# Performance work log

Hardware: AMD Instinct MI355X
Metric: run time of the kernel (lower is better)

## Reference

```python
import jax, jax.numpy as jnp
import numpy as np

B, T, V, E, H = 64, 512, 8192, 1024, 2048


def setup_inputs() -> dict:
    key = jax.random.key(0)
    k = jax.random.split(key, 8)
    idx = jax.random.randint(k[0], (B, T), 0, V)
    targets = jax.random.randint(k[1], (B, T), 0, V)
    s = 0.02
    W_E = jax.random.normal(k[2], (V, E), jnp.float32) * s
    start = jnp.zeros((1, H), jnp.float32)
    W_xh = jax.random.normal(k[3], (E + H, H), jnp.float32) * s  # Linear(E+H -> H)
    b_xh = jnp.zeros((H,), jnp.float32)
    W_head = jax.random.normal(k[4], (H, V), jnp.float32) * s
    b_head = jnp.zeros((V,), jnp.float32)
    return {"idx": idx, "targets": targets, "W_E": W_E, "start": start,
            "W_xh": W_xh, "b_xh": b_xh, "W_head": W_head, "b_head": b_head}


def reference(idx, targets, W_E, start, W_xh, b_xh, W_head, b_head):
    b, t = idx.shape
    emb = W_E[idx]  # [B, T, E]
    # split concat-linear: cat([x,h]) @ W_xh == x @ Wx + h @ Wh (same math)
    Wx, Wh = W_xh[:E], W_xh[E:]
    xproj = jnp.einsum('bte,eh->bth', emb, Wx) + b_xh  # precompute input part

    def step(h_prev, xp_t):
        h_t = jnp.tanh(xp_t + h_prev @ Wh)
        return h_t, h_t

    h0 = jnp.broadcast_to(start, (b, H))
    _, hs = jax.lax.scan(step, h0, jnp.swapaxes(xproj, 0, 1))  # [T, B, H]
    hidden = jnp.swapaxes(hs, 0, 1)  # [B, T, H]
    logits = jnp.einsum('bth,hv->btv', hidden, W_head) + b_head

    # cross entropy with ignore_index=-1
    logp = jax.nn.log_softmax(logits, axis=-1)
    mask = targets != -1
    tsafe = jnp.where(mask, targets, 0)
    nll = -jnp.take_along_axis(logp, tsafe[..., None], axis=-1)[..., 0]
    loss = jnp.sum(nll * mask) / jnp.maximum(jnp.sum(mask), 1)
    return logits, loss
```

## Files before the change

### kernel.cpp

```cpp
#include <hip/hip_runtime.h>
#include <hip/hip_bf16.h>
#include <math.h>
#include <stdint.h>

#define Bb 64
#define Tt 512
#define Vv 8192
#define Ee 1024
#define Hh 2048

typedef unsigned short u16;
typedef unsigned long long u64;
typedef __attribute__((ext_vector_type(8))) short bf16x8;
typedef __attribute__((ext_vector_type(8))) _Float16 f16x8;
typedef __attribute__((ext_vector_type(4))) float f32x4;

__device__ __forceinline__ u16 f2b(float f) {
  unsigned u = __float_as_uint(f);
  u += 0x7FFF + ((u >> 16) & 1);
  return (u16)(u >> 16);
}
__device__ __forceinline__ float b2f(u16 h) {
  return __uint_as_float(((unsigned)h) << 16);
}
__device__ __forceinline__ u16 f2h_bits(float f) {
  union { _Float16 h; u16 u; } c;
  c.h = (_Float16)f;
  return c.u;
}
__device__ __forceinline__ u64 pack4(u16 a, u16 b, u16 c, u16 d) {
  return (u64)a | ((u64)b << 16) | ((u64)c << 32) | ((u64)d << 48);
}

__device__ __forceinline__ void gload16f(f16x8& dst, const void* addr) {
  asm volatile("global_load_dwordx4 %0, %1, off sc1"
               : "=v"(dst) : "v"(addr) : "memory");
}

__device__ __forceinline__ void gll16(const u16* g, const u16* l) {
  __builtin_amdgcn_global_load_lds((__attribute__((address_space(1))) void*)g,
                                   (__attribute__((address_space(3))) void*)l, 16, 0, 0);
}

__device__ __forceinline__ float wave_max(float v) {
  #pragma unroll
  for (int d = 32; d; d >>= 1) v = fmaxf(v, __shfl_xor(v, d, 64));
  return v;
}
__device__ __forceinline__ float wave_sum(float v) {
  #pragma unroll
  for (int d = 32; d; d >>= 1) v += __shfl_xor(v, d, 64);
  return v;
}


__global__ __launch_bounds__(256)
void embed_cast_f16(const float* __restrict__ WE, const int* __restrict__ idx,
                    u16* __restrict__ emb) {
  const int m = blockIdx.x;
  const int row = idx[m];
  const float4 v = ((const float4*)(WE + (size_t)row * Ee))[threadIdx.x];
  ushort4 o;
  o.x = f2h_bits(v.x); o.y = f2h_bits(v.y);
  o.z = f2h_bits(v.z); o.w = f2h_bits(v.w);
  ((ushort4*)(emb + (size_t)m * Ee))[threadIdx.x] = o;
}

__global__ __launch_bounds__(256)
void transpose_cast(const float* __restrict__ src, u16* __restrict__ dst,
                    int R, int C) {
  __shared__ float tile[32][33];
  const int bi = blockIdx.x;
  const int bj = blockIdx.y;
  const int tid = threadIdx.x;
  const int r  = tid >> 3;
  const int c4 = (tid & 7) * 4;
  float4 v = *(const float4*)(src + (size_t)(bj * 32 + r) * C + bi * 32 + c4);
  tile[r][c4 + 0] = v.x; tile[r][c4 + 1] = v.y;
  tile[r][c4 + 2] = v.z; tile[r][c4 + 3] = v.w;
  __syncthreads();
  ushort4 o;
  o.x = f2b(tile[c4 + 0][r]); o.y = f2b(tile[c4 + 1][r]);
  o.z = f2b(tile[c4 + 2][r]); o.w = f2b(tile[c4 + 3][r]);
  *(ushort4*)(dst + (size_t)(bi * 32 + r) * R + bj * 32 + c4) = o;
}

__global__ __launch_bounds__(256)
void transpose_cast_f16(const float* __restrict__ src, u16* __restrict__ dst,
                        int R, int C) {
  __shared__ float tile[32][33];
  const int bi = blockIdx.x;
  const int bj = blockIdx.y;
  const int tid = threadIdx.x;
  const int r  = tid >> 3;
  const int c4 = (tid & 7) * 4;
  float4 v = *(const float4*)(src + (size_t)(bj * 32 + r) * C + bi * 32 + c4);
  tile[r][c4 + 0] = v.x; tile[r][c4 + 1] = v.y;
  tile[r][c4 + 2] = v.z; tile[r][c4 + 3] = v.w;
  __syncthreads();
  ushort4 o;
  o.x = f2h_bits(tile[c4 + 0][r]); o.y = f2h_bits(tile[c4 + 1][r]);
  o.z = f2h_bits(tile[c4 + 2][r]); o.w = f2h_bits(tile[c4 + 3][r]);
  *(ushort4*)(dst + (size_t)(bi * 32 + r) * R + bj * 32 + c4) = o;
}

__global__ __launch_bounds__(256)
void h0_init(const float* __restrict__ start, u16* __restrict__ hbuf) {
  const int b = blockIdx.x;
  #pragma unroll
  for (int j = 0; j < 8; ++j) {
    int n = threadIdx.x * 8 + j;
    hbuf[(size_t)b * 2048 + n] = f2h_bits(start[n]);
  }
}

template <int MODE, int F16>
__global__ __launch_bounds__(256, 2)
void gemm_bt(const u16* __restrict__ A, const u16* __restrict__ Bt,
             const float* __restrict__ bias, void* __restrict__ outp,
             float* __restrict__ pm, float* __restrict__ ps,
             int M, int N, int K) {
  __shared__ u16 ldsA[128 * 32];
  __shared__ u16 ldsB[128 * 32];
  __shared__ float sm_[2][2][64];
  __shared__ float ss_[2][2][64];
  const int tid = threadIdx.x;
  const int lane = tid & 63;
  const int w = tid >> 6;
  const int wr = w >> 1, wc = w & 1;

  const int nwg = gridDim.x * gridDim.y;
  const int lin = blockIdx.y * gridDim.x + blockIdx.x;
  const int swz = (lin & 7) * (nwg >> 3) + (lin >> 3);
  const int bm = swz % gridDim.x;
  const int bn = swz / gridDim.x;

  const int srow = w * 32 + (lane >> 2);
  const int scol = (lane & 3) * 8;
  const u16* a0 = A + (size_t)(bm * 128 + srow) * K + scol;
  const u16* b0 = Bt + (size_t)(bn * 128 + srow) * K + scol;
  u16* lA0 = ldsA + w * 1024;
  u16* lA1 = ldsA + w * 1024 + 512;
  u16* lB0 = ldsB + w * 1024;
  u16* lB1 = ldsB + w * 1024 + 512;

  f32x4 acc[4][4];
  #pragma unroll
  for (int m = 0; m < 4; ++m)
    #pragma unroll
    for (int n = 0; n < 4; ++n)
      acc[m][n] = (f32x4){0.f, 0.f, 0.f, 0.f};

  const int nk = K >> 5;
  for (int kt = 0; kt < nk; ++kt) {
    __syncthreads();
    const u16* ak = a0 + kt * 32;
    const u16* bk = b0 + kt * 32;
    gll16(ak, lA0);
    gll16(ak + 16 * (size_t)K, lA1);
    gll16(bk, lB0);
    gll16(bk + 16 * (size_t)K, lB1);
    __syncthreads();
    bf16x8 af[4], bfr[4];
    #pragma unroll
    for (int i = 0; i < 4; ++i) {
      af[i]  = *(const bf16x8*)&ldsA[(wr * 64 + i * 16 + (lane & 15)) * 32 + (lane >> 4) * 8];
      bfr[i] = *(const bf16x8*)&ldsB[(wc * 64 + i * 16 + (lane & 15)) * 32 + (lane >> 4) * 8];
    }
    #pragma unroll
    for (int m = 0; m < 4; ++m)
      #pragma unroll
      for (int n = 0; n < 4; ++n) {
        if (F16) {
          acc[m][n] = __builtin_amdgcn_mfma_f32_16x16x32_f16(
              *(const f16x8*)&af[m], *(const f16x8*)&bfr[n], acc[m][n], 0, 0, 0);
        } else {
          acc[m][n] = __builtin_amdgcn_mfma_f32_16x16x32_bf16(af[m], bfr[n], acc[m][n], 0, 0, 0);
        }
      }
  }

  const int r0 = bm * 128 + wr * 64 + (lane >> 4) * 4;
  const int c0 = bn * 128 + wc * 64 + (lane & 15);

  if (MODE == 0) {
    float bv[4];
    #pragma unroll
    for (int n = 0; n < 4; ++n) bv[n] = bias[c0 + n * 16];
    #pragma unroll
    for (int m = 0; m < 4; ++m) {
      #pragma unroll
      for (int q = 0; q < 4; ++q) {
        const int row = r0 + m * 16 + q;
        float v[4];
        float mx = -1e30f;
        #pragma unroll
        for (int n = 0; n < 4; ++n) {
          v[n] = acc[m][n][q] + bv[n];
          ((float*)outp)[(size_t)row * N + c0 + n * 16] = v[n];
          mx = fmaxf(mx, v[n]);
        }
        #pragma unroll
        for (int d = 1; d < 16; d <<= 1) mx = fmaxf(mx, __shfl_xor(mx, d, 64));
        float se = 0.f;
        #pragma unroll
        for (int n = 0; n < 4; ++n) se += expf(v[n] - mx);
        #pragma unroll
        for (int d = 1; d < 16; d <<= 1) se += __shfl_xor(se, d, 64);
        if ((lane & 15) == 0) {
          const int rl = m * 16 + (lane >> 4) * 4 + q;
          sm_[wc][wr][rl] = mx;
          ss_[wc][wr][rl] = se;
        }
      }
    }
    __syncthreads();
    if (w < 2) {
      float m0 = sm_[0][w][lane], m1 = sm_[1][w][lane];
      float s0 = ss_[0][w][lane], s1 = ss_[1][w][lane];
      float Mx = fmaxf(m0, m1);
      float S = s0 * expf(m0 - Mx) + s1 * expf(m1 - Mx);
      const int row = bm * 128 + w * 64 + lane;
      pm[(size_t)row * 64 + bn] = Mx;
      ps[(size_t)row * 64 + bn] = S;
    }
  } else {
    #pragma unroll
    for (int n = 0; n < 4; ++n) {
      const int col = c0 + n * 16;
      const float bv = bias[col];
      #pragma unroll
      for (int m = 0; m < 4; ++m) {
        #pragma unroll
        for (int q = 0; q < 4; ++q) {
          const int row = r0 + m * 16 + q;
          float v = acc[m][n][q] + bv;
          const int b = row >> 9, t = row & 511;
          ((u16*)outp)[((size_t)t * Bb + b) * N + col] = f2b(v);
        }
      }
    }
  }
}

__global__ __launch_bounds__(512, 2)
void rnn_scan(const u16* __restrict__ WhT, const u16* __restrict__ xp,
              u16* __restrict__ hbuf, u16* __restrict__ hidden,
              unsigned* __restrict__ sync) {
  __shared__ u16 whi[65536];
  __shared__ float red[4096];

  const int bid = blockIdx.x;
  const int g = bid >> 6;
  const int colg = bid & 63;
  const int rowbase = g * 16;
  const int col0 = colg * 32;
  const int tid = threadIdx.x;
  const int lane = tid & 63;
  const int w = tid >> 6;

  for (int i = tid; i < 8192; i += 512) {
    const int ch = i & 3;
    const int cl = (i >> 2) & 15;
    const int kt = (i >> 6) & 63;
    const int c2 = (i >> 12) & 1;
    bf16x8 v = *(const bf16x8*)(WhT + (size_t)(col0 + c2 * 16 + cl) * 2048 + kt * 32 + ch * 8);
    *(bf16x8*)&whi[(size_t)(c2 * 64 + kt) * 512 + ch * 128 + cl * 8] = v;
  }
  __syncthreads();

  unsigned* cnt = sync + g * 64;
  bool dead = false;
  const int hrow = rowbase + (lane & 15);

  ushort4 xv = {0, 0, 0, 0};
  if (w < 2)
    xv = *(const ushort4*)(xp + (size_t)hrow * 2048 + col0 + w * 16 + (lane >> 4) * 4);

  for (int t = 0; t < Tt; ++t) {
    const u16* hp = hbuf + (size_t)(t & 1) * (64 * 2048);
    u16*       hn = hbuf + (size_t)((t + 1) & 1) * (64 * 2048);

    f16x8 qh[8];
    const u16* hb = hp + (size_t)hrow * 2048 + (lane >> 4) * 8;
    #pragma unroll
    for (int kt = 0; kt < 8; ++kt)
      gload16f(qh[kt], hb + (w * 8 + kt) * 32);
    asm volatile("s_waitcnt vmcnt(0)" ::: "memory");
    __builtin_amdgcn_sched_barrier(0);

    f32x4 a0 = (f32x4){0.f, 0.f, 0.f, 0.f};
    f32x4 a1 = (f32x4){0.f, 0.f, 0.f, 0.f};
    #pragma unroll
    for (int kt = 0; kt < 8; ++kt) {
      const int ktG = w * 8 + kt;
      f16x8 w0 = *(const f16x8*)&whi[(size_t)(0 * 64 + ktG) * 512 + (lane >> 4) * 128 + (lane & 15) * 8];
      f16x8 w1 = *(const f16x8*)&whi[(size_t)(1 * 64 + ktG) * 512 + (lane >> 4) * 128 + (lane & 15) * 8];
      a0 = __builtin_amdgcn_mfma_f32_16x16x32_f16(w0, qh[kt], a0, 0, 0, 0);
      a1 = __builtin_amdgcn_mfma_f32_16x16x32_f16(w1, qh[kt], a1, 0, 0, 0);
    }

    *(f32x4*)&red[(w) * 256 + lane * 4]     = a0;
    *(f32x4*)&red[(8 + w) * 256 + lane * 4] = a1;
    __syncthreads();

    if (w < 2) {
      f32x4 ac = (f32x4){0.f, 0.f, 0.f, 0.f};
      #pragma unroll
      for (int j = 0; j < 8; ++j)
        ac += *(const f32x4*)&red[(w * 8 + j) * 256 + lane * 4];
      const int cl0 = (lane >> 4) * 4;
      u16 hf[4], hbv[4];
      #pragma unroll
      for (int qq = 0; qq < 4; ++qq) {
        float v = tanhf(ac[qq] + b2f(((const u16*)&xv)[qq]));
        hf[qq]  = f2h_bits(v);
        hbv[qq] = f2b(v);
      }
      u64 ph = pack4(hf[0], hf[1], hf[2], hf[3]);
      u64 pb = pack4(hbv[0], hbv[1], hbv[2], hbv[3]);
      u16* hd = hn + (size_t)hrow * 2048 + col0 + w * 16 + cl0;
      __hip_atomic_store((u64*)hd, ph, __ATOMIC_RELAXED, __HIP_MEMORY_SCOPE_AGENT);
      *(u64*)(hidden + ((size_t)hrow * Tt + t) * Hh + col0 + w * 16 + cl0) = pb;
    }

    __syncthreads();
    if (w < 2 && t + 1 < Tt)
      xv = *(const ushort4*)(xp + ((size_t)(t + 1) * Bb + hrow) * 2048 + col0 + w * 16 + (lane >> 4) * 4);
    if (tid == 0) {
      unsigned old = __hip_atomic_fetch_add(cnt, 1u, __ATOMIC_RELAXED, __HIP_MEMORY_SCOPE_AGENT);
      if (old != (unsigned)(t * 64 + 63) && !dead) {
        unsigned polls = 0;
        while (__hip_atomic_load(cnt, __ATOMIC_RELAXED, __HIP_MEMORY_SCOPE_AGENT)
               < (unsigned)((t + 1) * 64)) {
          if (++polls > 4000000u) { dead = true; break; }
        }
      }
    }
    __syncthreads();
  }
}


__global__ __launch_bounds__(256)
void nll_from_partials(const float* __restrict__ pm, const float* __restrict__ ps,
                       const float* __restrict__ logits, const int* __restrict__ tgt,
                       float* __restrict__ nll) {
  const int r = blockIdx.x * 4 + (threadIdx.x >> 6);
  const int lane = threadIdx.x & 63;
  float m = pm[(size_t)r * 64 + lane];
  float s = ps[(size_t)r * 64 + lane];
  float M = wave_max(m);
  float S = wave_sum(s * expf(m - M));
  if (lane == 0) {
    const int tg = tgt[r];
    float o = 0.f;
    if (tg != -1) o = M + logf(S) - logits[(size_t)r * Vv + tg];
    nll[r] = o;
  }
}

__global__ __launch_bounds__(256)
void loss_reduce(const float* __restrict__ nll, const int* __restrict__ tgt,
                 float* __restrict__ out) {
  const int tid = threadIdx.x;
  float s = 0.f, c = 0.f;
  for (int i = tid; i < Bb * Tt; i += 256) {
    s += nll[i];
    c += (tgt[i] != -1) ? 1.f : 0.f;
  }
  s = wave_sum(s);
  c = wave_sum(c);
  __shared__ float as_[4], ac_[4];
  const int w = tid >> 6;
  if ((tid & 63) == 0) { as_[w] = s; ac_[w] = c; }
  __syncthreads();
  if (tid == 0) {
    float S = as_[0] + as_[1] + as_[2] + as_[3];
    float C = ac_[0] + ac_[1] + ac_[2] + ac_[3];
    out[0] = S / fmaxf(C, 1.f);
  }
}


extern "C" void kernel_launch(void* const* d_in, const int* in_sizes, int n_in,
                              void* d_out, int out_size, void* d_ws, size_t ws_size,
                              hipStream_t stream) {
  const int*   idx    = (const int*)d_in[0];
  const int*   tgt    = (const int*)d_in[1];
  const float* W_E    = (const float*)d_in[2];
  const float* start  = (const float*)d_in[3];
  const float* W_xh   = (const float*)d_in[4];
  const float* b_xh   = (const float*)d_in[5];
  const float* W_head = (const float*)d_in[6];
  const float* b_head = (const float*)d_in[7];

  char* ws = (char*)d_ws;
  u16*      emb16  = (u16*)(ws);
  u16*      hidden = (u16*)(ws);
  u16*      xproj  = (u16*)(ws + (size_t)128 * 1024 * 1024);
  float*    pm     = (float*)(ws + (size_t)128 * 1024 * 1024);
  float*    ps     = (float*)(ws + (size_t)136 * 1024 * 1024);
  u16*      WheadT = (u16*)(ws + (size_t)256 * 1024 * 1024);
  u16*      WhT    = (u16*)(ws + (size_t)288 * 1024 * 1024);
  u16*      WxT16  = (u16*)(ws + (size_t)304 * 1024 * 1024);
  u16*      hbuf   = (u16*)(ws + (size_t)312 * 1024 * 1024);
  float*    nll    = (float*)(ws + (size_t)313 * 1024 * 1024);
  unsigned* sync   = (unsigned*)(ws + (size_t)313 * 1024 * 1024 + 128 * 1024);

  embed_cast_f16<<<Bb * Tt, 256, 0, stream>>>(W_E, idx, emb16);
  transpose_cast_f16<<<dim3(Hh / 32, Ee / 32), 256, 0, stream>>>(W_xh, WxT16, Ee, Hh);
  transpose_cast_f16<<<dim3(Hh / 32, Hh / 32), 256, 0, stream>>>(W_xh + (size_t)Ee * Hh, WhT, Hh, Hh);
  transpose_cast<<<dim3(Vv / 32, Hh / 32), 256, 0, stream>>>(W_head, WheadT, Hh, Vv);
  h0_init<<<Bb, 256, 0, stream>>>(start, hbuf);
  hipMemsetAsync(sync, 0, 1024, stream);

  gemm_bt<1, 1><<<dim3(256, 16), 256, 0, stream>>>(emb16, WxT16, b_xh, xproj, nullptr, nullptr,
                                                   Bb * Tt, Hh, 1024);

  rnn_scan<<<256, 512, 0, stream>>>(WhT, xproj, hbuf, hidden, sync);

  gemm_bt<0, 0><<<dim3(256, 64), 256, 0, stream>>>(hidden, WheadT, b_head, d_out, pm, ps,
                                                   Bb * Tt, Vv, 2048);

  nll_from_partials<<<Bb * Tt / 4, 256, 0, stream>>>(pm, ps, (const float*)d_out, tgt, nll);
  loss_reduce<<<1, 256, 0, stream>>>(nll, tgt, (float*)d_out + ((size_t)out_size - 1));
}
```

Baseline: 4.376 ms.

## Spread RNN epilogue across all waves and switch head GEMM to fp16

The RNN scan epilogue now has all 8 waves each handle one output element, doing the reduction, tanh and stores, instead of only 2 waves handling four elements each. This is meant to shorten the serialized per-step tail. The spin-wait adds s_sleep to reduce polling pressure. The hidden states and the transposed head weights are now stored as fp16 rather than bf16, and the head GEMM uses the f16 template variant. In exchange the epilogue issues many narrow 2-byte stores instead of 8-byte packed ones.

After: 4.391 ms. About the same (+0.3%).

```diff
diff --git a/kernel.cpp b/kernel.cpp
--- a/kernel.cpp
+++ b/kernel.cpp
@@ -28,13 +28,14 @@
   c.h = (_Float16)f;
   return c.u;
 }
-__device__ __forceinline__ u64 pack4(u16 a, u16 b, u16 c, u16 d) {
-  return (u64)a | ((u64)b << 16) | ((u64)c << 32) | ((u64)d << 48);
-}
 
 __device__ __forceinline__ void gload16f(f16x8& dst, const void* addr) {
   asm volatile("global_load_dwordx4 %0, %1, off sc1"
                : "=v"(dst) : "v"(addr) : "memory");
+}
+__device__ __forceinline__ void gstore2_sc1(void* addr, unsigned val) {
+  asm volatile("global_store_short %0, %1, off sc1"
+               :: "v"(addr), "v"(val) : "memory");
 }
 
 __device__ __forceinline__ void gll16(const u16* g, const u16* l) {
@@ -64,25 +65,6 @@
   o.x = f2h_bits(v.x); o.y = f2h_bits(v.y);
   o.z = f2h_bits(v.z); o.w = f2h_bits(v.w);
   ((ushort4*)(emb + (size_t)m * Ee))[threadIdx.x] = o;
-}
-
-__global__ __launch_bounds__(256)
-void transpose_cast(const float* __restrict__ src, u16* __restrict__ dst,
-                    int R, int C) {
-  __shared__ float tile[32][33];
-  const int bi = blockIdx.x;
-  const int bj = blockIdx.y;
-  const int tid = threadIdx.x;
-  const int r  = tid >> 3;
-  const int c4 = (tid & 7) * 4;
-  float4 v = *(const float4*)(src + (size_t)(bj * 32 + r) * C + bi * 32 + c4);
-  tile[r][c4 + 0] = v.x; tile[r][c4 + 1] = v.y;
-  tile[r][c4 + 2] = v.z; tile[r][c4 + 3] = v.w;
-  __syncthreads();
-  ushort4 o;
-  o.x = f2b(tile[c4 + 0][r]); o.y = f2b(tile[c4 + 1][r]);
-  o.z = f2b(tile[c4 + 2][r]); o.w = f2b(tile[c4 + 3][r]);
-  *(ushort4*)(dst + (size_t)(bi * 32 + r) * R + bj * 32 + c4) = o;
 }
 
 __global__ __launch_bounds__(256)
@@ -273,9 +255,14 @@
   bool dead = false;
   const int hrow = rowbase + (lane & 15);
 
-  ushort4 xv = {0, 0, 0, 0};
-  if (w < 2)
-    xv = *(const ushort4*)(xp + (size_t)hrow * 2048 + col0 + w * 16 + (lane >> 4) * 4);
+  const int ev = w * 64 + lane;
+  const int ef = ev >> 8;
+  const int ep = ev & 255;
+  const int el = ep >> 2, eq = ep & 3;
+  const int erow = rowbase + (el & 15);
+  const int ecol = col0 + ef * 16 + ((el >> 4) << 2) + eq;
+
+  u16 xv16 = xp[(size_t)erow * 2048 + ecol];
 
   for (int t = 0; t < Tt; ++t) {
     const u16* hp = hbuf + (size_t)(t & 1) * (64 * 2048);
@@ -304,36 +291,28 @@
     *(f32x4*)&red[(8 + w) * 256 + lane * 4] = a1;
     __syncthreads();
 
-    if (w < 2) {
-      f32x4 ac = (f32x4){0.f, 0.f, 0.f, 0.f};
+    {
+      float s = 0.f;
       #pragma unroll
       for (int j = 0; j < 8; ++j)
-        ac += *(const f32x4*)&red[(w * 8 + j) * 256 + lane * 4];
-      const int cl0 = (lane >> 4) * 4;
-      u16 hf[4], hbv[4];
-      #pragma unroll
-      for (int qq = 0; qq < 4; ++qq) {
-        float v = tanhf(ac[qq] + b2f(((const u16*)&xv)[qq]));
-        hf[qq]  = f2h_bits(v);
-        hbv[qq] = f2b(v);
-      }
-      u64 ph = pack4(hf[0], hf[1], hf[2], hf[3]);
-      u64 pb = pack4(hbv[0], hbv[1], hbv[2], hbv[3]);
-      u16* hd = hn + (size_t)hrow * 2048 + col0 + w * 16 + cl0;
-      __hip_atomic_store((u64*)hd, ph, __ATOMIC_RELAXED, __HIP_MEMORY_SCOPE_AGENT);
-      *(u64*)(hidden + ((size_t)hrow * Tt + t) * Hh + col0 + w * 16 + cl0) = pb;
-    }
-
-    __syncthreads();
-    if (w < 2 && t + 1 < Tt)
-      xv = *(const ushort4*)(xp + ((size_t)(t + 1) * Bb + hrow) * 2048 + col0 + w * 16 + (lane >> 4) * 4);
+        s += red[(ef * 8 + j) * 256 + ep];
+      float hv = tanhf(s + b2f(xv16));
+      u16 hf = f2h_bits(hv);
+      gstore2_sc1(hn + (size_t)erow * 2048 + ecol, (unsigned)hf);
+      hidden[((size_t)erow * Tt + t) * Hh + ecol] = hf;
+    }
+
+    __syncthreads();
+    if (t + 1 < Tt)
+      xv16 = xp[((size_t)(t + 1) * Bb + erow) * 2048 + ecol];
     if (tid == 0) {
       unsigned old = __hip_atomic_fetch_add(cnt, 1u, __ATOMIC_RELAXED, __HIP_MEMORY_SCOPE_AGENT);
       if (old != (unsigned)(t * 64 + 63) && !dead) {
         unsigned polls = 0;
         while (__hip_atomic_load(cnt, __ATOMIC_RELAXED, __HIP_MEMORY_SCOPE_AGENT)
                < (unsigned)((t + 1) * 64)) {
-          if (++polls > 4000000u) { dead = true; break; }
+          __builtin_amdgcn_s_sleep(1);
+          if (++polls > 1000000u) { dead = true; break; }
         }
       }
     }
@@ -411,7 +390,7 @@
   embed_cast_f16<<<Bb * Tt, 256, 0, stream>>>(W_E, idx, emb16);
   transpose_cast_f16<<<dim3(Hh / 32, Ee / 32), 256, 0, stream>>>(W_xh, WxT16, Ee, Hh);
   transpose_cast_f16<<<dim3(Hh / 32, Hh / 32), 256, 0, stream>>>(W_xh + (size_t)Ee * Hh, WhT, Hh, Hh);
-  transpose_cast<<<dim3(Vv / 32, Hh / 32), 256, 0, stream>>>(W_head, WheadT, Hh, Vv);
+  transpose_cast_f16<<<dim3(Vv / 32, Hh / 32), 256, 0, stream>>>(W_head, WheadT, Hh, Vv);
   h0_init<<<Bb, 256, 0, stream>>>(start, hbuf);
   hipMemsetAsync(sync, 0, 1024, stream);
 
@@ -420,7 +399,7 @@
 
   rnn_scan<<<256, 512, 0, stream>>>(WhT, xproj, hbuf, hidden, sync);
 
-  gemm_bt<0, 0><<<dim3(256, 64), 256, 0, stream>>>(hidden, WheadT, b_head, d_out, pm, ps,
+  gemm_bt<0, 1><<<dim3(256, 64), 256, 0, stream>>>(hidden, WheadT, b_head, d_out, pm, ps,
                                                    Bb * Tt, Vv, 2048);
 
   nll_from_partials<<<Bb * Tt / 4, 256, 0, stream>>>(pm, ps, (const float*)d_out, tgt, nll);
```
